# Kernel tuning notes

Measured on AMD Instinct MI355X. Metric: run time of the kernel, lower is better.

Reference implementation:

```python
import jax, jax.numpy as jnp
import numpy as np

DIM = 512; NH = 8; HD = DIM // NH; WS = 28; N = WS * WS; H3 = (DIM * 4) // 3; EPS = 1e-6; B = 16


def _rel_pos_index(H, W):
    # static numpy computation of Swin-style relative position index [N, N]
    coords = np.stack(np.meshgrid(np.arange(H), np.arange(W), indexing='ij')).reshape(2, -1)
    rel = (coords[:, :, None] - coords[:, None, :]).transpose(1, 2, 0)
    rel[..., 0] += H - 1
    rel[..., 1] += W - 1
    rel[..., 0] *= 2 * W - 1
    return rel.sum(-1)

RPI = jnp.asarray(_rel_pos_index(WS, WS))  # [N, N] int


def adaptive_ln(x, w, b, a1w, a1b, a2w, a2b):
    # x: [B,C,H,W]; adapt params from global-avg-pooled 1x1 convs (== matmuls)
    C = x.shape[1]
    pooled = x.mean(axis=(2, 3))                      # [B,C]
    h = jax.nn.relu(pooled @ a1w.T + a1b)             # [B,C/4]
    ad = h @ a2w.T + a2b                              # [B,2C]
    aw = ad[:, :C][:, :, None, None]
    ab = ad[:, C:][:, :, None, None]
    u = x.mean(axis=1, keepdims=True)
    s = ((x - u) ** 2).mean(axis=1, keepdims=True)
    xn = (x - u) * jax.lax.rsqrt(s + EPS)
    return (w[None, :, None, None] * (1.0 + aw)) * xn + (b[None, :, None, None] + ab)


def dwconv(x, w, b):
    y = jax.lax.conv_general_dilated(x, w, (1, 1), 'SAME', feature_group_count=x.shape[1],
                                     dimension_numbers=('NCHW', 'OIHW', 'NCHW'))
    return y + b[None, :, None, None]


def conv1x1(x, w, b):
    return jnp.einsum('bchw,oc->bohw', x, w) + b[None, :, None, None]


def _forward(x, face_priors, n1_w, n1_b, n1_a1w, n1_a1b, n1_a2w, n1_a2b,
             n2_w, n2_b, n2_a1w, n2_a1b, n2_a2w, n2_a2b,
             qkv_w, qkv_b, rpb_table, struct_prior, proj_w, proj_b,
             eye_w, eye_b, nose_w, nose_b, mouth_w, mouth_b,
             fusion_w, fusion_b, gate1_w, gate1_b, gate2_w, gate2_b,
             es1_w, es1_b, es2_w, es2_b, em1_w, em1_b, em2_w, em2_b,
             el1_w, el1_b, el2_w, el2_b, router_w, router_b):
    Bx, C, H, W = x.shape
    n = H * W
    shortcut = x
    xa = adaptive_ln(x, n1_w, n1_b, n1_a1w, n1_a1b, n1_a2w, n1_a2b)
    # --- TripletFaceAttention ---
    xf = xa.reshape(Bx, C, n).transpose(0, 2, 1)                     # [B,N,C]
    qkv = (xf @ qkv_w.T + qkv_b).reshape(Bx, n, 3, NH, HD).transpose(2, 0, 3, 1, 4)
    q, k, v = qkv[0], qkv[1], qkv[2]                                 # [B,h,N,d]
    attn = jnp.einsum('bhnd,bhmd->bhnm', q, k) * (HD ** -0.5)
    attn = attn + struct_prior                                       # learned structure prior [1,h,N,N]
    rpb = rpb_table[RPI]                                             # [N,N,h]
    attn = attn + jnp.transpose(rpb, (2, 0, 1))[None]                # + relative position bias
    attn = attn * face_priors[:, None]                               # multiplicative face mask
    attn = jax.nn.softmax(attn, axis=-1)
    o = jnp.einsum('bhnm,bhmd->bhnd', attn, v).transpose(0, 2, 1, 3).reshape(Bx, n, C)
    o = o @ proj_w.T + proj_b
    x = shortcut + o.transpose(0, 2, 1).reshape(Bx, C, H, W)
    # --- FaceTokenMixer ---
    xn2 = adaptive_ln(x, n2_w, n2_b, n2_a1w, n2_a1b, n2_a2w, n2_a2b)
    cat = jnp.concatenate([dwconv(xn2, eye_w, eye_b),
                           dwconv(xn2, nose_w, nose_b),
                           dwconv(xn2, mouth_w, mouth_b)], axis=1)   # [B,3C,H,W]
    g = jax.nn.sigmoid(conv1x1(jax.nn.relu(conv1x1(xn2, gate1_w, gate1_b)), gate2_w, gate2_b))
    x = x + conv1x1(cat * g, fusion_w, fusion_b)
    # --- EfficientMLP (3-expert MoE, soft routing) ---
    r = jax.nn.softmax(x.mean(axis=(2, 3)) @ router_w.T + router_b, axis=-1)  # [B,3]
    def expert(w1, b1, w2, b2):
        return conv1x1(jax.nn.gelu(conv1x1(x, w1, b1), approximate=False), w2, b2)
    out = (r[:, 0, None, None, None] * expert(es1_w, es1_b, es2_w, es2_b)
           + r[:, 1, None, None, None] * expert(em1_w, em1_b, em2_w, em2_b)
           + r[:, 2, None, None, None] * expert(el1_w, el1_b, el2_w, el2_b))
    return x + out


def setup_inputs() -> dict:
    ks = iter(jax.random.split(jax.random.key(0), 64))
    def rn(shape, s=0.02):
        return jax.random.normal(next(ks), shape, jnp.float32) * s
    d = {}
    d['x'] = jax.random.normal(next(ks), (B, DIM, WS, WS), jnp.float32)
    d['face_priors'] = jax.random.uniform(next(ks), (B, N, N), jnp.float32)
    for p in ('n1', 'n2'):
        d[p + '_w'] = jnp.ones((DIM,), jnp.float32)
        d[p + '_b'] = jnp.zeros((DIM,), jnp.float32)
        d[p + '_a1w'] = rn((DIM // 4, DIM)); d[p + '_a1b'] = jnp.zeros((DIM // 4,), jnp.float32)
        d[p + '_a2w'] = rn((2 * DIM, DIM // 4)); d[p + '_a2b'] = jnp.zeros((2 * DIM,), jnp.float32)
    d['qkv_w'] = rn((3 * DIM, DIM)); d['qkv_b'] = jnp.zeros((3 * DIM,), jnp.float32)
    d['rpb_table'] = rn(((2 * WS - 1) ** 2, NH))
    d['struct_prior'] = rn((1, NH, N, N))
    d['proj_w'] = rn((DIM, DIM)); d['proj_b'] = jnp.zeros((DIM,), jnp.float32)
    d['eye_w'] = rn((DIM, 1, 3, 3)); d['eye_b'] = jnp.zeros((DIM,), jnp.float32)
    d['nose_w'] = rn((DIM, 1, 5, 5)); d['nose_b'] = jnp.zeros((DIM,), jnp.float32)
    d['mouth_w'] = rn((DIM, 1, 7, 7)); d['mouth_b'] = jnp.zeros((DIM,), jnp.float32)
    d['fusion_w'] = rn((DIM, 3 * DIM)); d['fusion_b'] = jnp.zeros((DIM,), jnp.float32)
    d['gate1_w'] = rn((DIM // 4, DIM)); d['gate1_b'] = jnp.zeros((DIM // 4,), jnp.float32)
    d['gate2_w'] = rn((3 * DIM, DIM // 4)); d['gate2_b'] = jnp.zeros((3 * DIM,), jnp.float32)
    for e in ('es', 'em', 'el'):
        d[e + '1_w'] = rn((H3, DIM)); d[e + '1_b'] = jnp.zeros((H3,), jnp.float32)
        d[e + '2_w'] = rn((DIM, H3)); d[e + '2_b'] = jnp.zeros((DIM,), jnp.float32)
    d['router_w'] = rn((3, DIM)); d['router_b'] = jnp.zeros((3,), jnp.float32)
    return d


def reference(x, face_priors, n1_w, n1_b, n1_a1w, n1_a1b, n1_a2w, n1_a2b,
              n2_w, n2_b, n2_a1w, n2_a1b, n2_a2w, n2_a2b,
              qkv_w, qkv_b, rpb_table, struct_prior, proj_w, proj_b,
              eye_w, eye_b, nose_w, nose_b, mouth_w, mouth_b,
              fusion_w, fusion_b, gate1_w, gate1_b, gate2_w, gate2_b,
              es1_w, es1_b, es2_w, es2_b, em1_w, em1_b, em2_w, em2_b,
              el1_w, el1_b, el2_w, el2_b, router_w, router_b):
    return _forward(x, face_priors, n1_w, n1_b, n1_a1w, n1_a1b, n1_a2w, n1_a2b,
                    n2_w, n2_b, n2_a1w, n2_a1b, n2_a2w, n2_a2b,
                    qkv_w, qkv_b, rpb_table, struct_prior, proj_w, proj_b,
                    eye_w, eye_b, nose_w, nose_b, mouth_w, mouth_b,
                    fusion_w, fusion_b, gate1_w, gate1_b, gate2_w, gate2_b,
                    es1_w, es1_b, es2_w, es2_b, em1_w, em1_b, em2_w, em2_b,
                    el1_w, el1_b, el2_w, el2_b, router_w, router_b)
```

## Files before the change

### kernel.cpp

```cpp
#include <hip/hip_runtime.h>
#include <math.h>


#define NPIX 784
#define CDIM 512
#define NHEAD 8
#define C3 1536

typedef unsigned int uint;
typedef unsigned short ushort;
typedef float f32x4 __attribute__((ext_vector_type(4)));
typedef __bf16 bf16x8 __attribute__((ext_vector_type(8)));
typedef __bf16 bf16x2 __attribute__((ext_vector_type(2)));

#define OFF_XPM ((size_t)0)
#define OFF_W   ((size_t)3211264)
#define OFF_R2  ((size_t)5324288)
#define OFF_VBF ((size_t)14958080)
#define OFF_OBF ((size_t)18169344)
#define OFF_X2  ((size_t)21380608)
#define OFF_X3  ((size_t)27803136)
#define OFF_PL  ((size_t)34225664)
#define OFF_AD  ((size_t)34233856)
#define OFF_RB  ((size_t)34250240)
#define OFF_US  ((size_t)34250288)
#define OFF_RS  ((size_t)34262832)
#define OFF_E2C ((size_t)34275392)

#define WOFF_QKV 0
#define WOFF_PROJ 786432
#define WOFF_G1  1048576
#define WOFF_G2  1114112
#define WOFF_FUS 1310720
#define WOFF_E1  2097152

__device__ __forceinline__ ushort f2bf(float f) {
  __bf16 h = (__bf16)f;
  return __builtin_bit_cast(ushort, h);
}
__device__ __forceinline__ unsigned pack2bf(float lo, float hi) {
  bf16x2 v = {(__bf16)lo, (__bf16)hi};
  return __builtin_bit_cast(unsigned, v);
}
__device__ __forceinline__ float bf2f(ushort u) {
  unsigned x = ((unsigned)u) << 16;
  return __builtin_bit_cast(float, x);
}
__device__ __forceinline__ void unpack4bf(uint2 v, float* o) {
  o[0] = bf2f((ushort)(v.x & 0xffffu)); o[1] = bf2f((ushort)(v.x >> 16));
  o[2] = bf2f((ushort)(v.y & 0xffffu)); o[3] = bf2f((ushort)(v.y >> 16));
}

__global__ __launch_bounds__(64) void pool_mean_k(const float* __restrict__ x,
                                                  float* __restrict__ pooled) {
  int c = blockIdx.x, b = blockIdx.y;
  const float* row = x + ((size_t)b * CDIM + c) * NPIX;
  float s = 0.f;
  for (int i = threadIdx.x; i < NPIX; i += 64) s += row[i];
  #pragma unroll
  for (int off = 32; off; off >>= 1) s += __shfl_down(s, off);
  if (threadIdx.x == 0) pooled[b * CDIM + c] = s * (1.f / NPIX);
}

__global__ __launch_bounds__(256) void adapt_mlp_k(const float* __restrict__ pooled,
                                                   const float* __restrict__ a1w,
                                                   const float* __restrict__ a1b,
                                                   const float* __restrict__ a2w,
                                                   const float* __restrict__ a2b,
                                                   float* __restrict__ ad) {
  int b = blockIdx.x, tid = threadIdx.x;
  __shared__ float pl[CDIM];
  __shared__ float hh[128];
  for (int i = tid; i < CDIM; i += 256) pl[i] = pooled[b * CDIM + i];
  __syncthreads();
  if (tid < 128) {
    const float* w = a1w + (size_t)tid * CDIM;
    float a = a1b[tid];
    for (int k = 0; k < CDIM; ++k) a += w[k] * pl[k];
    hh[tid] = fmaxf(a, 0.f);
  }
  __syncthreads();
  for (int o = tid; o < 1024; o += 256) {
    const float* w = a2w + (size_t)o * 128;
    float a = a2b[o];
    for (int k = 0; k < 128; ++k) a += w[k] * hh[k];
    ad[b * 1024 + o] = a;
  }
}

template <int STATS>
__global__ __launch_bounds__(256) void ln_pm_k(const float* __restrict__ x,
                                               const float* __restrict__ w,
                                               const float* __restrict__ bias,
                                               const float* __restrict__ ad,
                                               ushort* __restrict__ out,
                                               float* __restrict__ ust,
                                               float* __restrict__ rstp) {
  int b = blockIdx.y;
  int p0 = blockIdx.x * 32;
  int tid = threadIdx.x;
  int px = tid & 31, cg = tid >> 5;
  int p = p0 + px;
  bool valid = p < NPIX;
  const float* xb = x + (size_t)b * CDIM * NPIX;
  float s = 0.f, s2 = 0.f;
  if (valid) {
    for (int c = cg * 64; c < cg * 64 + 64; ++c) {
      float v = xb[(size_t)c * NPIX + p];
      s += v; s2 += v * v;
    }
  }
  __shared__ float rs[8][32], rq[8][32], us[32], vs[32];
  rs[cg][px] = s; rq[cg][px] = s2;
  __syncthreads();
  if (tid < 32) {
    float ts = 0.f, ts2 = 0.f;
    #pragma unroll
    for (int g = 0; g < 8; ++g) { ts += rs[g][tid]; ts2 += rq[g][tid]; }
    float u = ts * (1.f / CDIM);
    float var = ts2 * (1.f / CDIM) - u * u;
    float rv = rsqrtf(var + 1e-6f);
    us[tid] = u; vs[tid] = rv;
    if (STATS && p0 + tid < NPIX) {
      ust[(size_t)b * NPIX + p0 + tid] = u;
      rstp[(size_t)b * NPIX + p0 + tid] = rv;
    }
  }
  __syncthreads();
  if (valid) {
    float u = us[px], rv = vs[px];
    const float* aw = ad + (size_t)b * 1024;
    const float* ab = aw + CDIM;
    ushort* ob = out + ((size_t)(b * NPIX + p)) * CDIM + cg * 64;
    for (int cb = 0; cb < 64; cb += 8) {
      int c = cg * 64 + cb;
      float vv[8];
      #pragma unroll
      for (int q = 0; q < 8; ++q) {
        float v = xb[(size_t)(c + q) * NPIX + p];
        vv[q] = w[c + q] * (1.f + aw[c + q]) * ((v - u) * rv) + (bias[c + q] + ab[c + q]);
      }
      uint4 o = {pack2bf(vv[0], vv[1]), pack2bf(vv[2], vv[3]),
                 pack2bf(vv[4], vv[5]), pack2bf(vv[6], vv[7])};
      *(uint4*)(ob + cb) = o;
    }
  }
}

struct CvtDesc {
  const float* s[11];
  ushort* d[11];
  int rows[11], sk[11], dk[11], ds[11], rr[11];
};
__global__ __launch_bounds__(256) void cvt_w_k(CvtDesc D) {
  int seg = blockIdx.y;
  int sk = D.sk[seg], dk = D.dk[seg], ds = D.ds[seg], rr = D.rr[seg];
  int total = D.rows[seg] * dk;
  const float* s = D.s[seg];
  ushort* d = D.d[seg];
  for (int i = blockIdx.x * 256 + threadIdx.x; i < total; i += gridDim.x * 256) {
    int r = i / dk, cc = i - r * dk;
    d[(size_t)r * ds + cc] = (cc < sk && r < rr) ? f2bf(s[(size_t)r * sk + cc]) : (ushort)0;
  }
}

__global__ __launch_bounds__(256) void sprpb_k(const float* __restrict__ sp,
                                               const float* __restrict__ rpb,
                                               ushort* __restrict__ out) {
  const int q = blockIdx.x, h = blockIdx.y;
  const int i1 = q / 28, j1 = q - i1 * 28;
  const float* src = sp + ((size_t)h * NPIX + q) * NPIX;
  ushort* dst = out + ((size_t)h * NPIX + q) * NPIX;
  for (int m = threadIdx.x; m < NPIX; m += 256) {
    int i2 = m / 28, j2 = m - i2 * 28;
    float rv = rpb[(size_t)((i1 - i2 + 27) * 55 + (j1 - j2 + 27)) * NHEAD + h];
    dst[m] = f2bf(src[m] + rv);
  }
}

__global__ __launch_bounds__(256) void fpcvt_k(const float* __restrict__ fp,
                                               ushort* __restrict__ out) {
  size_t i = (size_t)blockIdx.x * 256 + threadIdx.x;
  float4 v = *((const float4*)fp + i);
  ushort4 o;
  o.x = f2bf(v.x); o.y = f2bf(v.y); o.z = f2bf(v.z); o.w = f2bf(v.w);
  *((ushort4*)out + i) = o;
}

__global__ __launch_bounds__(512) void biaseff_k(const float* __restrict__ rbuf,
                                                 const float* __restrict__ b0,
                                                 const float* __restrict__ b1,
                                                 const float* __restrict__ b2,
                                                 const float* __restrict__ a0,
                                                 const float* __restrict__ a1,
                                                 const float* __restrict__ a2,
                                                 float* __restrict__ be,
                                                 float* __restrict__ e1bcat) {
  int b = blockIdx.x;
  if (b < 16) {
    int n = threadIdx.x;
    be[b * 512 + n] = rbuf[b * 3] * b0[n] + rbuf[b * 3 + 1] * b1[n] + rbuf[b * 3 + 2] * b2[n];
  } else {
    for (int i = threadIdx.x; i < 2112; i += 512) {
      int e = i / 704, r = i - e * 704;
      e1bcat[i] = (r < 682) ? (e == 0 ? a0 : e == 1 ? a1 : a2)[r] : 0.f;
    }
  }
}

template <int ORIENT, int EPI>
__global__ __launch_bounds__(256) void mgemm_k(const ushort* __restrict__ X,
                                               const ushort* __restrict__ Wt,
                                               const float* __restrict__ bias,
                                               const float* __restrict__ resid,
                                               const float* __restrict__ scales,
                                               void* __restrict__ OutV,
                                               int Ks, int Nreal, int Nstore) {
  const int bid = blockIdx.x;
  const int xcd = bid & 7;
  const int i = bid >> 3;
  const int mt_local = i % 14;
  const int nt = i / 14;
  const int m0 = (xcd * 14 + mt_local) * 112;
  const int n0 = nt * 128;
  const int bb = m0 / NPIX;
  const int t = threadIdx.x;
  const int w = t >> 6, lane = t & 63, c = lane & 15, g = lane >> 4;
  __shared__ ushort Xs[7168];
  __shared__ ushort Ws[8192];
  f32x4 acc[7][2];
  #pragma unroll
  for (int mi = 0; mi < 7; ++mi)
    #pragma unroll
    for (int ni = 0; ni < 2; ++ni) acc[mi][ni] = (f32x4){0.f, 0.f, 0.f, 0.f};

  for (int k0 = 0; k0 < Ks; k0 += 64) {
    for (int ii = t; ii < 896; ii += 256) {
      int m = ii >> 3, kg = ii & 7;
      uint4 v = *(const uint4*)(X + (size_t)(m0 + m) * Ks + k0 + kg * 8);
      *(uint4*)&Xs[m * 64 + ((kg ^ (m & 7)) << 3)] = v;
    }
    for (int ii = t; ii < 1024; ii += 256) {
      int n = ii >> 3, kg = ii & 7;
      uint4 v = {0u, 0u, 0u, 0u};
      if (n0 + n < Nreal) v = *(const uint4*)(Wt + (size_t)(n0 + n) * Ks + k0 + kg * 8);
      *(uint4*)&Ws[n * 64 + ((kg ^ (n & 7)) << 3)] = v;
    }
    __syncthreads();
    #pragma unroll
    for (int kc = 0; kc < 2; ++kc) {
      bf16x8 xf[7], wf[2];
      #pragma unroll
      for (int mi = 0; mi < 7; ++mi) {
        int m = mi * 16 + c;
        xf[mi] = *(const bf16x8*)&Xs[m * 64 + (((kc * 4 + g) ^ (m & 7)) << 3)];
      }
      #pragma unroll
      for (int ni = 0; ni < 2; ++ni) {
        int n = w * 32 + ni * 16 + c;
        wf[ni] = *(const bf16x8*)&Ws[n * 64 + (((kc * 4 + g) ^ (n & 7)) << 3)];
      }
      #pragma unroll
      for (int mi = 0; mi < 7; ++mi)
        #pragma unroll
        for (int ni = 0; ni < 2; ++ni)
          acc[mi][ni] = (ORIENT == 0)
            ? __builtin_amdgcn_mfma_f32_16x16x32_bf16(wf[ni], xf[mi], acc[mi][ni], 0, 0, 0)
            : __builtin_amdgcn_mfma_f32_16x16x32_bf16(xf[mi], wf[ni], acc[mi][ni], 0, 0, 0);
    }
    __syncthreads();
  }

  if (ORIENT == 0) {
    ushort* Ob = (ushort*)OutV;
    const int nbq = n0 + w * 32;
    float bi[2][4];
    #pragma unroll
    for (int ni = 0; ni < 2; ++ni)
      #pragma unroll
      for (int j = 0; j < 4; ++j) {
        int n = nbq + ni * 16 + g * 4 + j;
        bi[ni][j] = (n < Nreal) ? bias[n] : 0.f;
      }
    #pragma unroll
    for (int mi = 0; mi < 7; ++mi) {
      int m = m0 + mi * 16 + c;
      #pragma unroll
      for (int ni = 0; ni < 2; ++ni) {
        int nb = nbq + ni * 16 + g * 4;
        if (nb >= Nstore) continue;
        float v[4];
        #pragma unroll
        for (int j = 0; j < 4; ++j) v[j] = acc[mi][ni][j] + bi[ni][j];
        if (EPI == 1) {
          #pragma unroll
          for (int j = 0; j < 4; ++j) v[j] = fmaxf(v[j], 0.f);
        } else if (EPI == 2) {
          #pragma unroll
          for (int j = 0; j < 4; ++j)
            v[j] = 0.5f * v[j] * (1.f + erff(v[j] * 0.70710678118654752f));
        } else if (EPI == 3) {
          uint2 cm = *(const uint2*)&Ob[(size_t)m * Nstore + nb];
          float cf[4];
          unpack4bf(cm, cf);
          #pragma unroll
          for (int j = 0; j < 4; ++j)
            v[j] = (1.f / (1.f + __expf(-v[j]))) * cf[j];
        } else if (EPI == 5) {
          int e = nb / 704; e = (e > 2) ? 2 : e;
          float sc = scales[bb * 3 + e];
          #pragma unroll
          for (int j = 0; j < 4; ++j)
            v[j] = 0.5f * v[j] * (1.f + erff(v[j] * 0.70710678118654752f)) * sc;
        }
        uint2 o = {pack2bf(v[0], v[1]), pack2bf(v[2], v[3])};
        *(uint2*)&Ob[(size_t)m * Nstore + nb] = o;
      }
    }
  } else {
    const int prow = m0 - bb * NPIX;
    float* Ob = (float*)OutV + (size_t)bb * CDIM * NPIX;
    const float* Rb = resid + (size_t)bb * CDIM * NPIX;
    float sc = (EPI == 4 && scales) ? scales[bb * 3] : 1.f;
    #pragma unroll
    for (int ni = 0; ni < 2; ++ni) {
      int n = n0 + w * 32 + ni * 16 + c;
      float bv = (EPI == 5) ? bias[(size_t)bb * CDIM + n] : bias[n];
      #pragma unroll
      for (int mi = 0; mi < 7; ++mi) {
        int p = prow + mi * 16 + g * 4;
        size_t off = (size_t)n * NPIX + p;
        float4 r = *(const float4*)&Rb[off];
        f32x4 a = acc[mi][ni];
        float4 o = {r.x + sc * (a[0] + bv), r.y + sc * (a[1] + bv),
                    r.z + sc * (a[2] + bv), r.w + sc * (a[3] + bv)};
        *(float4*)&Ob[off] = o;
      }
    }
  }
}

__global__ __launch_bounds__(256) void vtr_k(const ushort* __restrict__ qkvbf,
                                             ushort* __restrict__ vbf) {
  const int p0 = blockIdx.x * 64, c0 = blockIdx.y * 64, b = blockIdx.z;
  __shared__ ushort T[64][72];
  for (int idx = threadIdx.x; idx < 512; idx += 256) {
    int pl = idx >> 3, cq = idx & 7;
    int p = p0 + pl;
    uint4 v = {0u, 0u, 0u, 0u};
    if (p < NPIX)
      v = *(const uint4*)(qkvbf + (size_t)(b * NPIX + p) * C3 + 1024 + c0 + cq * 8);
    *(uint4*)&T[pl][cq * 8] = v;
  }
  __syncthreads();
  for (int idx = threadIdx.x; idx < 512; idx += 256) {
    int cl = idx >> 3, pq = idx & 7;
    if (p0 + pq * 8 < NPIX) {
      ushort tmp[8];
      #pragma unroll
      for (int i = 0; i < 8; ++i) tmp[i] = T[pq * 8 + i][cl];
      *(uint4*)(vbf + ((size_t)(b * CDIM + c0 + cl)) * NPIX + p0 + pq * 8) =
          *(const uint4*)&tmp[0];
    }
  }
}

__global__ __launch_bounds__(256) void tr_cvt_k(const float* __restrict__ src,
                                                ushort* __restrict__ dst) {
  const int p0 = blockIdx.x * 64, c0 = blockIdx.y * 64, b = blockIdx.z;
  __shared__ ushort T[64][72];
  const float* sb = src + (size_t)b * CDIM * NPIX;
  for (int idx = threadIdx.x; idx < 4096; idx += 256) {
    int ci = idx >> 6, pj = idx & 63;
    int p = p0 + pj;
    T[pj][ci] = (p < NPIX) ? f2bf(sb[(size_t)(c0 + ci) * NPIX + p]) : (ushort)0;
  }
  __syncthreads();
  for (int idx = threadIdx.x; idx < 512; idx += 256) {
    int pj = idx >> 3, cq = idx & 7;
    int p = p0 + pj;
    if (p < NPIX) {
      uint4 v = *(const uint4*)&T[pj][cq * 8];
      *(uint4*)(dst + ((size_t)(b * NPIX + p)) * CDIM + c0 + cq * 8) = v;
    }
  }
}

__global__ __launch_bounds__(256) void attn_mfma_k(const ushort* __restrict__ qkvbf,
                                                   const ushort* __restrict__ vbf,
                                                   const ushort* __restrict__ sprpb,
                                                   const ushort* __restrict__ fpb,
                                                   ushort* __restrict__ obf) {
  const int bid = blockIdx.x;
  const int xcd = bid & 7;
  const int i = bid >> 3;
  const int b = xcd + 8 * (i / 56);
  const int r = i % 56;
  const int h = r & 7;
  const int qt = r >> 3;
  const int w = threadIdx.x >> 6, lane = threadIdx.x & 63;
  const int g = lane >> 4, c = lane & 15;
  const int q0 = qt * 128 + w * 32;
  if (q0 >= NPIX) return;
  const bool hasB = (q0 + 16) < NPIX;
  const int qA = q0 + c;
  const int qB = q0 + 16 + c;

  __shared__ uint BL[4][2][384];
  uint* bwA = BL[w][0];
  uint* bwB = BL[w][1];

  const ushort* qpA = qkvbf + (size_t)(b * NPIX + qA) * C3 + h * 64 + g * 8;
  const bf16x8 qfA0 = *(const bf16x8*)qpA;
  const bf16x8 qfA1 = *(const bf16x8*)(qpA + 32);
  bf16x8 qfB0 = qfA0, qfB1 = qfA1;
  if (hasB) {
    const ushort* qpB = qkvbf + (size_t)(b * NPIX + qB) * C3 + h * 64 + g * 8;
    qfB0 = *(const bf16x8*)qpB;
    qfB1 = *(const bf16x8*)(qpB + 32);
  }

  const ushort* kbase = qkvbf + (size_t)b * NPIX * C3 + 512 + h * 64 + g * 8;
  const ushort* vbase = vbf + ((size_t)b * CDIM + h * 64) * NPIX;
  const ushort* sprA = sprpb + ((size_t)h * NPIX + qA) * NPIX;
  const ushort* sprB = sprpb + ((size_t)h * NPIX + (hasB ? qB : qA)) * NPIX;
  const ushort* fpA = fpb + ((size_t)b * NPIX + qA) * NPIX;
  const ushort* fpB = fpb + ((size_t)b * NPIX + (hasB ? qB : qA)) * NPIX;

  f32x4 oA0 = {0.f, 0.f, 0.f, 0.f}, oA1 = oA0, oA2 = oA0, oA3 = oA0;
  f32x4 oB0 = oA0, oB1 = oA0, oB2 = oA0, oB3 = oA0;
  float MA = -1e30f, LA = 0.f, MB = -1e30f, LB = 0.f;

  for (int ms = 0; ms < 25; ++ms) {
    const int m0 = ms * 32;
    const bool full = (ms < 24);

    const ushort* kp = kbase + (size_t)(m0 + c) * C3;
    bf16x8 ka0 = *(const bf16x8*)kp;
    bf16x8 ka1 = *(const bf16x8*)(kp + 32);
    bf16x8 kb0 = ka0, kb1 = ka1;
    if (full) {
      const ushort* kp1 = kp + (size_t)16 * C3;
      kb0 = *(const bf16x8*)kp1;
      kb1 = *(const bf16x8*)(kp1 + 32);
    }

    f32x4 sA0 = {0.f, 0.f, 0.f, 0.f}, sA1 = sA0;
    sA0 = __builtin_amdgcn_mfma_f32_16x16x32_bf16(ka0, qfA0, sA0, 0, 0, 0);
    sA0 = __builtin_amdgcn_mfma_f32_16x16x32_bf16(ka1, qfA1, sA0, 0, 0, 0);
    if (full) {
      sA1 = __builtin_amdgcn_mfma_f32_16x16x32_bf16(kb0, qfA0, sA1, 0, 0, 0);
      sA1 = __builtin_amdgcn_mfma_f32_16x16x32_bf16(kb1, qfA1, sA1, 0, 0, 0);
    }

    float vA0[4], vA1[4];
    {
      float spv[4], fpv[4];
      unpack4bf(*(const uint2*)(sprA + m0 + g * 4), spv);
      unpack4bf(*(const uint2*)(fpA + m0 + g * 4), fpv);
      #pragma unroll
      for (int j = 0; j < 4; ++j) vA0[j] = fmaf(sA0[j], 0.125f, spv[j]) * fpv[j];
      if (full) {
        unpack4bf(*(const uint2*)(sprA + m0 + 16 + g * 4), spv);
        unpack4bf(*(const uint2*)(fpA + m0 + 16 + g * 4), fpv);
        #pragma unroll
        for (int j = 0; j < 4; ++j) vA1[j] = fmaf(sA1[j], 0.125f, spv[j]) * fpv[j];
      }
    }
    {
      float tm = fmaxf(fmaxf(vA0[0], vA0[1]), fmaxf(vA0[2], vA0[3]));
      if (full) tm = fmaxf(tm, fmaxf(fmaxf(vA1[0], vA1[1]), fmaxf(vA1[2], vA1[3])));
      tm = fmaxf(tm, __shfl_xor(tm, 16));
      tm = fmaxf(tm, __shfl_xor(tm, 32));
      if (__any(tm > MA)) {
        const float nM = fmaxf(MA, tm);
        const float fac = __expf(MA - nM);
        LA *= fac;
        #pragma unroll
        for (int j = 0; j < 4; ++j) { oA0[j] *= fac; oA1[j] *= fac; oA2[j] *= fac; oA3[j] *= fac; }
        MA = nM;
      }
      float p0v[4], p1v[4];
      float ps = 0.f;
      #pragma unroll
      for (int j = 0; j < 4; ++j) { p0v[j] = __expf(vA0[j] - MA); ps += p0v[j]; }
      if (full) {
        #pragma unroll
        for (int j = 0; j < 4; ++j) { p1v[j] = __expf(vA1[j] - MA); ps += p1v[j]; }
      }
      ps += __shfl_xor(ps, 16);
      ps += __shfl_xor(ps, 32);
      LA += ps;
      uint2 wlo, whi;
      wlo.x = pack2bf(p0v[0], p0v[1]);
      wlo.y = pack2bf(p0v[2], p0v[3]);
      whi.x = full ? pack2bf(p1v[0], p1v[1]) : 0u;
      whi.y = full ? pack2bf(p1v[2], p1v[3]) : 0u;
      *(uint2*)&bwA[lane * 6] = wlo;
      *(uint2*)&bwA[lane * 6 + 2] = whi;
    }

    if (hasB) {
      f32x4 sB0 = {0.f, 0.f, 0.f, 0.f}, sB1 = sB0;
      sB0 = __builtin_amdgcn_mfma_f32_16x16x32_bf16(ka0, qfB0, sB0, 0, 0, 0);
      sB0 = __builtin_amdgcn_mfma_f32_16x16x32_bf16(ka1, qfB1, sB0, 0, 0, 0);
      if (full) {
        sB1 = __builtin_amdgcn_mfma_f32_16x16x32_bf16(kb0, qfB0, sB1, 0, 0, 0);
        sB1 = __builtin_amdgcn_mfma_f32_16x16x32_bf16(kb1, qfB1, sB1, 0, 0, 0);
      }
      float vB0[4], vB1[4];
      {
        float spv[4], fpv[4];
        unpack4bf(*(const uint2*)(sprB + m0 + g * 4), spv);
        unpack4bf(*(const uint2*)(fpB + m0 + g * 4), fpv);
        #pragma unroll
        for (int j = 0; j < 4; ++j) vB0[j] = fmaf(sB0[j], 0.125f, spv[j]) * fpv[j];
        if (full) {
          unpack4bf(*(const uint2*)(sprB + m0 + 16 + g * 4), spv);
          unpack4bf(*(const uint2*)(fpB + m0 + 16 + g * 4), fpv);
          #pragma unroll
          for (int j = 0; j < 4; ++j) vB1[j] = fmaf(sB1[j], 0.125f, spv[j]) * fpv[j];
        }
      }
      float tm = fmaxf(fmaxf(vB0[0], vB0[1]), fmaxf(vB0[2], vB0[3]));
      if (full) tm = fmaxf(tm, fmaxf(fmaxf(vB1[0], vB1[1]), fmaxf(vB1[2], vB1[3])));
      tm = fmaxf(tm, __shfl_xor(tm, 16));
      tm = fmaxf(tm, __shfl_xor(tm, 32));
      if (__any(tm > MB)) {
        const float nM = fmaxf(MB, tm);
        const float fac = __expf(MB - nM);
        LB *= fac;
        #pragma unroll
        for (int j = 0; j < 4; ++j) { oB0[j] *= fac; oB1[j] *= fac; oB2[j] *= fac; oB3[j] *= fac; }
        MB = nM;
      }
      float p0v[4], p1v[4];
      float ps = 0.f;
      #pragma unroll
      for (int j = 0; j < 4; ++j) { p0v[j] = __expf(vB0[j] - MB); ps += p0v[j]; }
      if (full) {
        #pragma unroll
        for (int j = 0; j < 4; ++j) { p1v[j] = __expf(vB1[j] - MB); ps += p1v[j]; }
      }
      ps += __shfl_xor(ps, 16);
      ps += __shfl_xor(ps, 32);
      LB += ps;
      uint2 wlo, whi;
      wlo.x = pack2bf(p0v[0], p0v[1]);
      wlo.y = pack2bf(p0v[2], p0v[3]);
      whi.x = full ? pack2bf(p1v[0], p1v[1]) : 0u;
      whi.y = full ? pack2bf(p1v[2], p1v[3]) : 0u;
      *(uint2*)&bwB[lane * 6] = wlo;
      *(uint2*)&bwB[lane * 6 + 2] = whi;
    }

    const int f = g >> 1;
    const int slo = 32 * (g & 1) + c;
    uint2 blo = *(const uint2*)&bwA[slo * 6 + f * 2];
    uint2 bhi = *(const uint2*)&bwA[(slo + 16) * 6 + f * 2];
    uint4 bba = {blo.x, blo.y, bhi.x, bhi.y};
    const bf16x8 pfA = __builtin_bit_cast(bf16x8, bba);

    const ushort* vp = vbase + (size_t)c * NPIX + m0 + g * 8;
    bf16x8 vf0 = *(const bf16x8*)(vp);
    bf16x8 vf1 = *(const bf16x8*)(vp + (size_t)16 * NPIX);
    bf16x8 vf2 = *(const bf16x8*)(vp + (size_t)32 * NPIX);
    bf16x8 vf3 = *(const bf16x8*)(vp + (size_t)48 * NPIX);
    oA0 = __builtin_amdgcn_mfma_f32_16x16x32_bf16(vf0, pfA, oA0, 0, 0, 0);
    oA1 = __builtin_amdgcn_mfma_f32_16x16x32_bf16(vf1, pfA, oA1, 0, 0, 0);
    oA2 = __builtin_amdgcn_mfma_f32_16x16x32_bf16(vf2, pfA, oA2, 0, 0, 0);
    oA3 = __builtin_amdgcn_mfma_f32_16x16x32_bf16(vf3, pfA, oA3, 0, 0, 0);
    if (hasB) {
      uint2 clo = *(const uint2*)&bwB[slo * 6 + f * 2];
      uint2 chi = *(const uint2*)&bwB[(slo + 16) * 6 + f * 2];
      uint4 bbb = {clo.x, clo.y, chi.x, chi.y};
      const bf16x8 pfB = __builtin_bit_cast(bf16x8, bbb);
      oB0 = __builtin_amdgcn_mfma_f32_16x16x32_bf16(vf0, pfB, oB0, 0, 0, 0);
      oB1 = __builtin_amdgcn_mfma_f32_16x16x32_bf16(vf1, pfB, oB1, 0, 0, 0);
      oB2 = __builtin_amdgcn_mfma_f32_16x16x32_bf16(vf2, pfB, oB2, 0, 0, 0);
      oB3 = __builtin_amdgcn_mfma_f32_16x16x32_bf16(vf3, pfB, oB3, 0, 0, 0);
    }
  }

  {
    const float invL = 1.f / LA;
    ushort* dst = obf + (size_t)(b * NPIX + qA) * CDIM + h * 64 + g * 4;
    f32x4 ot[4] = {oA0, oA1, oA2, oA3};
    #pragma unroll
    for (int t2 = 0; t2 < 4; ++t2) {
      uint2 o = {pack2bf(ot[t2][0] * invL, ot[t2][1] * invL),
                 pack2bf(ot[t2][2] * invL, ot[t2][3] * invL)};
      *(uint2*)(dst + t2 * 16) = o;
    }
  }
  if (hasB) {
    const float invL = 1.f / LB;
    ushort* dst = obf + (size_t)(b * NPIX + qB) * CDIM + h * 64 + g * 4;
    f32x4 ot[4] = {oB0, oB1, oB2, oB3};
    #pragma unroll
    for (int t2 = 0; t2 < 4; ++t2) {
      uint2 o = {pack2bf(ot[t2][0] * invL, ot[t2][1] * invL),
                 pack2bf(ot[t2][2] * invL, ot[t2][3] * invL)};
      *(uint2*)(dst + t2 * 16) = o;
    }
  }
}

__device__ __forceinline__ float bf2f_s(ushort u) { return bf2f(u); }

template <int R>
__device__ __forceinline__ void conv_pass(const ushort* __restrict__ plane_ci,
                                          const float* __restrict__ wl_ci,
                                          float bv, int slot,
                                          ushort (*__restrict__ outb)[16], int ci) {
  constexpr int K = 2 * R + 1;
  float wreg[K * K];
  #pragma unroll
  for (int i = 0; i < K * K; ++i) wreg[i] = wl_ci[i];
  #pragma unroll
  for (int r7 = 0; r7 < 7; ++r7) {
    const int run = slot + r7 * 16;
    const int y = run >> 2, x0 = (run & 3) * 7;
    float acc[7];
    #pragma unroll
    for (int i = 0; i < 7; ++i) acc[i] = bv;
    #pragma unroll
    for (int dy = 0; dy < K; ++dy) {
      const ushort* rp = plane_ci + (y + 3 - R + dy) * 34 + (x0 + 3 - R);
      float win[7 + 2 * R];
      #pragma unroll
      for (int k = 0; k < 7 + 2 * R; ++k) win[k] = bf2f_s(rp[k]);
      #pragma unroll
      for (int i = 0; i < 7; ++i)
        #pragma unroll
        for (int k = 0; k < K; ++k)
          acc[i] = fmaf(win[i + k], wreg[dy * K + k], acc[i]);
    }
    #pragma unroll
    for (int i = 0; i < 7; ++i) outb[y * 28 + x0 + i][ci] = f2bf(acc[i]);
  }
}

__global__ __launch_bounds__(256) void dwln_k(const float* __restrict__ x2,
    const float* __restrict__ ust, const float* __restrict__ rst,
    const float* __restrict__ ad, const float* __restrict__ n2w,
    const float* __restrict__ n2b,
    const float* __restrict__ ew, const float* __restrict__ eb,
    const float* __restrict__ nw, const float* __restrict__ nb,
    const float* __restrict__ mw, const float* __restrict__ mb,
    ushort* __restrict__ cat) {
  const int cg = blockIdx.x, b = blockIdx.y;
  const int c0 = cg * 16;
  const int t = threadIdx.x;
  const int ci = t & 15, slot = t >> 4;

  __shared__ ushort plane[16][1156];
  __shared__ ushort outb[784][16];
  __shared__ float Wl[16 * 49];
  __shared__ float LWs[16], LBs[16];

  {
    uint* pz = (uint*)&plane[0][0];
    for (int i = t; i < 16 * 1156 / 2; i += 256) pz[i] = 0u;
  }
  if (t < 16) {
    int cc = c0 + t;
    float aw = ad[b * 1024 + cc], ab = ad[b * 1024 + 512 + cc];
    LWs[t] = n2w[cc] * (1.f + aw);
    LBs[t] = n2b[cc] + ab;
  }
  __syncthreads();

  {
    float uu[4], rr[4];
    #pragma unroll
    for (int j = 0; j < 4; ++j) {
      int p = t + j * 256;
      if (p < NPIX) {
        uu[j] = ust[(size_t)b * NPIX + p];
        rr[j] = rst[(size_t)b * NPIX + p];
      }
    }
    for (int cc = 0; cc < 16; ++cc) {
      const float* xp = x2 + ((size_t)(b * CDIM + c0 + cc)) * NPIX;
      float lw = LWs[cc], lb = LBs[cc];
      #pragma unroll
      for (int j = 0; j < 4; ++j) {
        int p = t + j * 256;
        if (p < NPIX) {
          int y = p / 28, xx2 = p - y * 28;
          plane[cc][(y + 3) * 34 + xx2 + 3] = f2bf(lw * (xp[p] - uu[j]) * rr[j] + lb);
        }
      }
    }
  }
  __syncthreads();

  #pragma unroll 1
  for (int cv = 0; cv < 3; ++cv) {
    const float* gw = (cv == 0) ? ew : (cv == 1) ? nw : mw;
    const float* gb = (cv == 0) ? eb : (cv == 1) ? nb : mb;
    const int K2 = (cv == 0) ? 9 : (cv == 1) ? 25 : 49;
    for (int i = t; i < 16 * K2; i += 256) {
      int cc = i / K2, k = i - cc * K2;
      Wl[cc * K2 + k] = gw[(size_t)(c0 + cc) * K2 + k];
    }
    __syncthreads();
    float bv = gb[c0 + ci];
    if (cv == 0)      conv_pass<1>(&plane[ci][0], &Wl[ci * 9],  bv, slot, outb, ci);
    else if (cv == 1) conv_pass<2>(&plane[ci][0], &Wl[ci * 25], bv, slot, outb, ci);
    else              conv_pass<3>(&plane[ci][0], &Wl[ci * 49], bv, slot, outb, ci);
    __syncthreads();
    for (int idx = t; idx < NPIX * 2; idx += 256) {
      int p = idx >> 1, half = idx & 1;
      uint4 v = *(const uint4*)&outb[p][half * 8];
      *(uint4*)(cat + ((size_t)(b * NPIX + p)) * C3 + cv * 512 + c0 + half * 8) = v;
    }
    __syncthreads();
  }
}

__global__ __launch_bounds__(64) void router_k(const float* __restrict__ pooled,
                                               const float* __restrict__ rw,
                                               const float* __restrict__ rb,
                                               float* __restrict__ r) {
  int b = blockIdx.x, lane = threadIdx.x;
  float a0 = 0.f, a1 = 0.f, a2 = 0.f;
  for (int k = lane; k < CDIM; k += 64) {
    float p = pooled[b * CDIM + k];
    a0 += rw[k] * p;
    a1 += rw[CDIM + k] * p;
    a2 += rw[2 * CDIM + k] * p;
  }
  #pragma unroll
  for (int off = 32; off; off >>= 1) {
    a0 += __shfl_down(a0, off);
    a1 += __shfl_down(a1, off);
    a2 += __shfl_down(a2, off);
  }
  if (lane == 0) {
    float l0 = a0 + rb[0], l1 = a1 + rb[1], l2 = a2 + rb[2];
    float mx = fmaxf(l0, fmaxf(l1, l2));
    float e0 = __expf(l0 - mx), e1 = __expf(l1 - mx), e2 = __expf(l2 - mx);
    float inv = 1.f / (e0 + e1 + e2);
    r[b * 3 + 0] = e0 * inv;
    r[b * 3 + 1] = e1 * inv;
    r[b * 3 + 2] = e2 * inv;
  }
}

extern "C" void kernel_launch(void* const* d_in, const int* in_sizes, int n_in,
                              void* d_out, int out_size, void* d_ws, size_t ws_size,
                              hipStream_t stream) {
  (void)in_sizes; (void)n_in; (void)out_size; (void)ws_size;
  const float* x         = (const float*)d_in[0];
  const float* fpri      = (const float*)d_in[1];
  const float* n1_w      = (const float*)d_in[2];
  const float* n1_b      = (const float*)d_in[3];
  const float* n1_a1w    = (const float*)d_in[4];
  const float* n1_a1b    = (const float*)d_in[5];
  const float* n1_a2w    = (const float*)d_in[6];
  const float* n1_a2b    = (const float*)d_in[7];
  const float* n2_w      = (const float*)d_in[8];
  const float* n2_b      = (const float*)d_in[9];
  const float* n2_a1w    = (const float*)d_in[10];
  const float* n2_a1b    = (const float*)d_in[11];
  const float* n2_a2w    = (const float*)d_in[12];
  const float* n2_a2b    = (const float*)d_in[13];
  const float* qkv_w     = (const float*)d_in[14];
  const float* qkv_b     = (const float*)d_in[15];
  const float* rpb_table = (const float*)d_in[16];
  const float* sprior    = (const float*)d_in[17];
  const float* proj_w    = (const float*)d_in[18];
  const float* proj_b    = (const float*)d_in[19];
  const float* eye_w     = (const float*)d_in[20];
  const float* eye_b     = (const float*)d_in[21];
  const float* nose_w    = (const float*)d_in[22];
  const float* nose_b    = (const float*)d_in[23];
  const float* mouth_w   = (const float*)d_in[24];
  const float* mouth_b   = (const float*)d_in[25];
  const float* fusion_w  = (const float*)d_in[26];
  const float* fusion_b  = (const float*)d_in[27];
  const float* gate1_w   = (const float*)d_in[28];
  const float* gate1_b   = (const float*)d_in[29];
  const float* gate2_w   = (const float*)d_in[30];
  const float* gate2_b   = (const float*)d_in[31];
  const float* e1w[3] = {(const float*)d_in[32], (const float*)d_in[36], (const float*)d_in[40]};
  const float* e1b[3] = {(const float*)d_in[33], (const float*)d_in[37], (const float*)d_in[41]};
  const float* e2w[3] = {(const float*)d_in[34], (const float*)d_in[38], (const float*)d_in[42]};
  const float* e2b[3] = {(const float*)d_in[35], (const float*)d_in[39], (const float*)d_in[43]};
  const float* router_w  = (const float*)d_in[44];
  const float* router_b  = (const float*)d_in[45];

  float* ws    = (float*)d_ws;
  ushort* xpm  = (ushort*)(ws + OFF_XPM);
  ushort* wb   = (ushort*)(ws + OFF_W);
  ushort* r2u  = (ushort*)(ws + OFF_R2);
  ushort* vbf  = (ushort*)(ws + OFF_VBF);
  ushort* obf  = (ushort*)(ws + OFF_OBF);
  float* x2    = ws + OFF_X2;
  float* x3    = ws + OFF_X3;
  float* pld   = ws + OFF_PL;
  float* adb   = ws + OFF_AD;
  float* rbuf  = ws + OFF_RB;
  float* ust   = ws + OFF_US;
  float* rst   = ws + OFF_RS;
  float* outp  = (float*)d_out;

  ushort* qkvw  = wb + WOFF_QKV;
  ushort* projw = wb + WOFF_PROJ;
  ushort* g1w   = wb + WOFF_G1;
  ushort* g2w   = wb + WOFF_G2;
  ushort* fusw  = wb + WOFF_FUS;
  ushort* e1cat = wb + WOFF_E1;
  ushort* e2cat = (ushort*)(ws + OFF_E2C);
  float* be     = adb;
  float* e1bcat = adb + 8192;

  ushort* fpbf   = (ushort*)x2;
  ushort* sprpbf = (ushort*)x3;

  CvtDesc D;
  auto seg = [&](int s2, const float* src, ushort* dst, int rows, int sk, int dk,
                 int ds, int rr) {
    D.s[s2] = src; D.d[s2] = dst; D.rows[s2] = rows; D.sk[s2] = sk;
    D.dk[s2] = dk; D.ds[s2] = ds; D.rr[s2] = rr;
  };
  seg(0, qkv_w,    qkvw,  1536, 512,  512,  512,  1536);
  seg(1, proj_w,   projw, 512,  512,  512,  512,  512);
  seg(2, gate1_w,  g1w,   128,  512,  512,  512,  128);
  seg(3, gate2_w,  g2w,   1536, 128,  128,  128,  1536);
  seg(4, fusion_w, fusw,  512,  1536, 1536, 1536, 512);
  for (int e = 0; e < 3; ++e) {
    seg(5 + e, e1w[e], e1cat + (size_t)e * 704 * 512, 704, 512, 512, 512, 682);
    seg(8 + e, e2w[e], e2cat + (size_t)e * 704,       512, 682, 704, 2112, 512);
  }
  cvt_w_k<<<dim3(512, 11), 256, 0, stream>>>(D);

  sprpb_k<<<dim3(NPIX, NHEAD), 256, 0, stream>>>(sprior, rpb_table, sprpbf);
  fpcvt_k<<<9604, 256, 0, stream>>>(fpri, fpbf);

  pool_mean_k<<<dim3(CDIM, 16), 64, 0, stream>>>(x, pld);
  adapt_mlp_k<<<16, 256, 0, stream>>>(pld, n1_a1w, n1_a1b, n1_a2w, n1_a2b, adb);
  ln_pm_k<0><<<dim3(25, 16), 256, 0, stream>>>(x, n1_w, n1_b, adb, xpm, nullptr, nullptr);

  mgemm_k<0, 0><<<1344, 256, 0, stream>>>(xpm, qkvw, qkv_b, nullptr, nullptr,
                                          r2u, 512, 1536, 1536);
  vtr_k<<<dim3(13, 8, 16), 256, 0, stream>>>(r2u, vbf);
  attn_mfma_k<<<896, 256, 0, stream>>>(r2u, vbf, sprpbf, fpbf, obf);
  mgemm_k<1, 4><<<448, 256, 0, stream>>>(obf, projw, proj_b, x, nullptr,
                                         x2, 512, 512, 512);

  pool_mean_k<<<dim3(CDIM, 16), 64, 0, stream>>>(x2, pld);
  adapt_mlp_k<<<16, 256, 0, stream>>>(pld, n2_a1w, n2_a1b, n2_a2w, n2_a2b, adb);
  ln_pm_k<1><<<dim3(25, 16), 256, 0, stream>>>(x2, n2_w, n2_b, adb, xpm, ust, rst);
  dwln_k<<<dim3(32, 16), 256, 0, stream>>>(x2, ust, rst, adb, n2_w, n2_b,
                                           eye_w, eye_b, nose_w, nose_b, mouth_w, mouth_b,
                                           r2u);
  mgemm_k<0, 1><<<112, 256, 0, stream>>>(xpm, g1w, gate1_b, nullptr, nullptr,
                                         obf, 512, 128, 128);
  mgemm_k<0, 3><<<1344, 256, 0, stream>>>(obf, g2w, gate2_b, nullptr, nullptr,
                                          r2u, 128, 1536, 1536);
  mgemm_k<1, 4><<<448, 256, 0, stream>>>(r2u, fusw, fusion_b, x2, nullptr,
                                         x3, 1536, 512, 512);

  tr_cvt_k<<<dim3(13, 8, 16), 256, 0, stream>>>(x3, xpm);
  pool_mean_k<<<dim3(CDIM, 16), 64, 0, stream>>>(x3, pld);
  router_k<<<16, 64, 0, stream>>>(pld, router_w, router_b, rbuf);
  biaseff_k<<<17, 512, 0, stream>>>(rbuf, e2b[0], e2b[1], e2b[2],
                                    e1b[0], e1b[1], e1b[2], be, e1bcat);
  mgemm_k<0, 5><<<1904, 256, 0, stream>>>(xpm, e1cat, e1bcat, nullptr, rbuf,
                                          r2u, 512, 2112, 2112);
  mgemm_k<1, 5><<<448, 256, 0, stream>>>(r2u, e2cat, be, x3, nullptr,
                                         outp, 2112, 512, 512);
}
```

Measured before the change: 816.7 us.

## Fuse pooling and bf16 transpose into GEMM epilogues; prefetch attention operands

```diff
diff --git a/kernel.cpp b/kernel.cpp
--- a/kernel.cpp
+++ b/kernel.cpp
@@ -59,7 +59,7 @@
   for (int i = threadIdx.x; i < NPIX; i += 64) s += row[i];
   #pragma unroll
   for (int off = 32; off; off >>= 1) s += __shfl_down(s, off);
-  if (threadIdx.x == 0) pooled[b * CDIM + c] = s * (1.f / NPIX);
+  if (threadIdx.x == 0) pooled[b * CDIM + c] = s;
 }
 
 __global__ __launch_bounds__(256) void adapt_mlp_k(const float* __restrict__ pooled,
@@ -71,7 +71,8 @@
   int b = blockIdx.x, tid = threadIdx.x;
   __shared__ float pl[CDIM];
   __shared__ float hh[128];
-  for (int i = tid; i < CDIM; i += 256) pl[i] = pooled[b * CDIM + i];
+  for (int i = tid; i < CDIM; i += 256)
+    pl[i] = pooled[b * CDIM + i] * (1.f / NPIX);
   __syncthreads();
   if (tid < 128) {
     const float* w = a1w + (size_t)tid * CDIM;
@@ -208,13 +209,15 @@
   }
 }
 
-template <int ORIENT, int EPI>
+template <int ORIENT, int EPI, int POOL, int DUALBF>
 __global__ __launch_bounds__(256) void mgemm_k(const ushort* __restrict__ X,
                                                const ushort* __restrict__ Wt,
                                                const float* __restrict__ bias,
                                                const float* __restrict__ resid,
                                                const float* __restrict__ scales,
                                                void* __restrict__ OutV,
+                                               float* __restrict__ pool_out,
+                                               ushort* __restrict__ pm_out,
                                                int Ks, int Nreal, int Nstore) {
   const int bid = blockIdx.x;
   const int xcd = bid & 7;
@@ -326,6 +329,7 @@
     for (int ni = 0; ni < 2; ++ni) {
       int n = n0 + w * 32 + ni * 16 + c;
       float bv = (EPI == 5) ? bias[(size_t)bb * CDIM + n] : bias[n];
+      float cs = 0.f;
       #pragma unroll
       for (int mi = 0; mi < 7; ++mi) {
         int p = prow + mi * 16 + g * 4;
@@ -335,6 +339,19 @@
         float4 o = {r.x + sc * (a[0] + bv), r.y + sc * (a[1] + bv),
                     r.z + sc * (a[2] + bv), r.w + sc * (a[3] + bv)};
         *(float4*)&Ob[off] = o;
+        if (POOL) cs += o.x + o.y + o.z + o.w;
+        if (DUALBF) {
+          size_t mg = (size_t)(m0 + mi * 16 + g * 4);
+          pm_out[mg * CDIM + n] = f2bf(o.x);
+          pm_out[(mg + 1) * CDIM + n] = f2bf(o.y);
+          pm_out[(mg + 2) * CDIM + n] = f2bf(o.z);
+          pm_out[(mg + 3) * CDIM + n] = f2bf(o.w);
+        }
+      }
+      if (POOL) {
+        cs += __shfl_xor(cs, 16);
+        cs += __shfl_xor(cs, 32);
+        if (g == 0) atomicAdd(pool_out + (size_t)bb * CDIM + n, cs);
       }
     }
   }
@@ -365,26 +382,9 @@
   }
 }
 
-__global__ __launch_bounds__(256) void tr_cvt_k(const float* __restrict__ src,
-                                                ushort* __restrict__ dst) {
-  const int p0 = blockIdx.x * 64, c0 = blockIdx.y * 64, b = blockIdx.z;
-  __shared__ ushort T[64][72];
-  const float* sb = src + (size_t)b * CDIM * NPIX;
-  for (int idx = threadIdx.x; idx < 4096; idx += 256) {
-    int ci = idx >> 6, pj = idx & 63;
-    int p = p0 + pj;
-    T[pj][ci] = (p < NPIX) ? f2bf(sb[(size_t)(c0 + ci) * NPIX + p]) : (ushort)0;
-  }
-  __syncthreads();
-  for (int idx = threadIdx.x; idx < 512; idx += 256) {
-    int pj = idx >> 3, cq = idx & 7;
-    int p = p0 + pj;
-    if (p < NPIX) {
-      uint4 v = *(const uint4*)&T[pj][cq * 8];
-      *(uint4*)(dst + ((size_t)(b * NPIX + p)) * CDIM + c0 + cq * 8) = v;
-    }
-  }
-}
+struct KFr { bf16x8 a0, a1, b0, b1; };
+struct VFr { bf16x8 v0, v1, v2, v3; };
+struct BFr { uint2 sl, fl, sh, fh; };
 
 __global__ __launch_bounds__(256) void attn_mfma_k(const ushort* __restrict__ qkvbf,
                                                    const ushort* __restrict__ vbf,
@@ -427,47 +427,77 @@
   const ushort* fpA = fpb + ((size_t)b * NPIX + qA) * NPIX;
   const ushort* fpB = fpb + ((size_t)b * NPIX + (hasB ? qB : qA)) * NPIX;
 
+  auto load_k = [&](int m0, bool tfull) -> KFr {
+    KFr k;
+    const ushort* kp = kbase + (size_t)(m0 + c) * C3;
+    k.a0 = *(const bf16x8*)kp;
+    k.a1 = *(const bf16x8*)(kp + 32);
+    const ushort* kp1 = kp + (tfull ? (size_t)16 * C3 : 0);
+    k.b0 = *(const bf16x8*)kp1;
+    k.b1 = *(const bf16x8*)(kp1 + 32);
+    return k;
+  };
+  auto load_v = [&](int m0) -> VFr {
+    VFr v;
+    const ushort* vp = vbase + (size_t)c * NPIX + m0 + g * 8;
+    v.v0 = *(const bf16x8*)(vp);
+    v.v1 = *(const bf16x8*)(vp + (size_t)16 * NPIX);
+    v.v2 = *(const bf16x8*)(vp + (size_t)32 * NPIX);
+    v.v3 = *(const bf16x8*)(vp + (size_t)48 * NPIX);
+    return v;
+  };
+  auto load_b = [&](const ushort* spr, const ushort* fp, int m0) -> BFr {
+    BFr x;
+    x.sl = *(const uint2*)(spr + m0 + g * 4);
+    x.fl = *(const uint2*)(fp + m0 + g * 4);
+    x.sh = *(const uint2*)(spr + m0 + 16 + g * 4);
+    x.fh = *(const uint2*)(fp + m0 + 16 + g * 4);
+    return x;
+  };
+
   f32x4 oA0 = {0.f, 0.f, 0.f, 0.f}, oA1 = oA0, oA2 = oA0, oA3 = oA0;
   f32x4 oB0 = oA0, oB1 = oA0, oB2 = oA0, oB3 = oA0;
   float MA = -1e30f, LA = 0.f, MB = -1e30f, LB = 0.f;
 
+  KFr kc = load_k(0, true);
+  VFr vc = load_v(0);
+  BFr bcA = load_b(sprA, fpA, 0);
+  BFr bcB = bcA;
+  if (hasB) bcB = load_b(sprB, fpB, 0);
+
   for (int ms = 0; ms < 25; ++ms) {
     const int m0 = ms * 32;
     const bool full = (ms < 24);
 
-    const ushort* kp = kbase + (size_t)(m0 + c) * C3;
-    bf16x8 ka0 = *(const bf16x8*)kp;
-    bf16x8 ka1 = *(const bf16x8*)(kp + 32);
-    bf16x8 kb0 = ka0, kb1 = ka1;
+    KFr kn; VFr vn; BFr bnA, bnB;
     if (full) {
-      const ushort* kp1 = kp + (size_t)16 * C3;
-      kb0 = *(const bf16x8*)kp1;
-      kb1 = *(const bf16x8*)(kp1 + 32);
+      const int nm0 = m0 + 32;
+      kn = load_k(nm0, ms + 1 < 24);
+      vn = load_v(nm0);
+      bnA = load_b(sprA, fpA, nm0);
+      if (hasB) bnB = load_b(sprB, fpB, nm0);
     }
 
     f32x4 sA0 = {0.f, 0.f, 0.f, 0.f}, sA1 = sA0;
-    sA0 = __builtin_amdgcn_mfma_f32_16x16x32_bf16(ka0, qfA0, sA0, 0, 0, 0);
-    sA0 = __builtin_amdgcn_mfma_f32_16x16x32_bf16(ka1, qfA1, sA0, 0, 0, 0);
+    sA0 = __builtin_amdgcn_mfma_f32_16x16x32_bf16(kc.a0, qfA0, sA0, 0, 0, 0);
+    sA0 = __builtin_amdgcn_mfma_f32_16x16x32_bf16(kc.a1, qfA1, sA0, 0, 0, 0);
     if (full) {
-      sA1 = __builtin_amdgcn_mfma_f32_16x16x32_bf16(kb0, qfA0, sA1, 0, 0, 0);
-      sA1 = __builtin_amdgcn_mfma_f32_16x16x32_bf16(kb1, qfA1, sA1, 0, 0, 0);
-    }
-
-    float vA0[4], vA1[4];
+      sA1 = __builtin_amdgcn_mfma_f32_16x16x32_bf16(kc.b0, qfA0, sA1, 0, 0, 0);
+      sA1 = __builtin_amdgcn_mfma_f32_16x16x32_bf16(kc.b1, qfA1, sA1, 0, 0, 0);
+    }
     {
+      float vA0[4], vA1[4];
       float spv[4], fpv[4];
-      unpack4bf(*(const uint2*)(sprA + m0 + g * 4), spv);
-      unpack4bf(*(const uint2*)(fpA + m0 + g * 4), fpv);
+      unpack4bf(bcA.sl, spv);
+      unpack4bf(bcA.fl, fpv);
       #pragma unroll
       for (int j = 0; j < 4; ++j) vA0[j] = fmaf(sA0[j], 0.125f, spv[j]) * fpv[j];
       if (full) {
-        unpack4bf(*(const uint2*)(sprA + m0 + 16 + g * 4), spv);
-        unpack4bf(*(const uint2*)(fpA + m0 + 16 + g * 4), fpv);
+        unpack4bf(bcA.sh, spv);
+        unpack4bf(bcA.fh, fpv);
         #pragma unroll
         for (int j = 0; j < 4; ++j) vA1[j] = fmaf(sA1[j], 0.125f, spv[j]) * fpv[j];
       }
-    }
-    {
       float tm = fmaxf(fmaxf(vA0[0], vA0[1]), fmaxf(vA0[2], vA0[3]));
       if (full) tm = fmaxf(tm, fmaxf(fmaxf(vA1[0], vA1[1]), fmaxf(vA1[2], vA1[3])));
       tm = fmaxf(tm, __shfl_xor(tm, 16));
@@ -502,25 +532,23 @@
 
     if (hasB) {
       f32x4 sB0 = {0.f, 0.f, 0.f, 0.f}, sB1 = sB0;
-      sB0 = __builtin_amdgcn_mfma_f32_16x16x32_bf16(ka0, qfB0, sB0, 0, 0, 0);
-      sB0 = __builtin_amdgcn_mfma_f32_16x16x32_bf16(ka1, qfB1, sB0, 0, 0, 0);
+      sB0 = __builtin_amdgcn_mfma_f32_16x16x32_bf16(kc.a0, qfB0, sB0, 0, 0, 0);
+      sB0 = __builtin_amdgcn_mfma_f32_16x16x32_bf16(kc.a1, qfB1, sB0, 0, 0, 0);
       if (full) {
-        sB1 = __builtin_amdgcn_mfma_f32_16x16x32_bf16(kb0, qfB0, sB1, 0, 0, 0);
-        sB1 = __builtin_amdgcn_mfma_f32_16x16x32_bf16(kb1, qfB1, sB1, 0, 0, 0);
+        sB1 = __builtin_amdgcn_mfma_f32_16x16x32_bf16(kc.b0, qfB0, sB1, 0, 0, 0);
+        sB1 = __builtin_amdgcn_mfma_f32_16x16x32_bf16(kc.b1, qfB1, sB1, 0, 0, 0);
       }
       float vB0[4], vB1[4];
-      {
-        float spv[4], fpv[4];
-        unpack4bf(*(const uint2*)(sprB + m0 + g * 4), spv);
-        unpack4bf(*(const uint2*)(fpB + m0 + g * 4), fpv);
+      float spv[4], fpv[4];
+      unpack4bf(bcB.sl, spv);
+      unpack4bf(bcB.fl, fpv);
+      #pragma unroll
+      for (int j = 0; j < 4; ++j) vB0[j] = fmaf(sB0[j], 0.125f, spv[j]) * fpv[j];
+      if (full) {
+        unpack4bf(bcB.sh, spv);
+        unpack4bf(bcB.fh, fpv);
         #pragma unroll
-        for (int j = 0; j < 4; ++j) vB0[j] = fmaf(sB0[j], 0.125f, spv[j]) * fpv[j];
-        if (full) {
-          unpack4bf(*(const uint2*)(sprB + m0 + 16 + g * 4), spv);
-          unpack4bf(*(const uint2*)(fpB + m0 + 16 + g * 4), fpv);
-          #pragma unroll
-          for (int j = 0; j < 4; ++j) vB1[j] = fmaf(sB1[j], 0.125f, spv[j]) * fpv[j];
-        }
+        for (int j = 0; j < 4; ++j) vB1[j] = fmaf(sB1[j], 0.125f, spv[j]) * fpv[j];
       }
       float tm = fmaxf(fmaxf(vB0[0], vB0[1]), fmaxf(vB0[2], vB0[3]));
       if (full) tm = fmaxf(tm, fmaxf(fmaxf(vB1[0], vB1[1]), fmaxf(vB1[2], vB1[3])));
@@ -560,26 +588,22 @@
     uint2 bhi = *(const uint2*)&bwA[(slo + 16) * 6 + f * 2];
     uint4 bba = {blo.x, blo.y, bhi.x, bhi.y};
     const bf16x8 pfA = __builtin_bit_cast(bf16x8, bba);
-
-    const ushort* vp = vbase + (size_t)c * NPIX + m0 + g * 8;
-    bf16x8 vf0 = *(const bf16x8*)(vp);
-    bf16x8 vf1 = *(const bf16x8*)(vp + (size_t)16 * NPIX);
-    bf16x8 vf2 = *(const bf16x8*)(vp + (size_t)32 * NPIX);
-    bf16x8 vf3 = *(const bf16x8*)(vp + (size_t)48 * NPIX);
-    oA0 = __builtin_amdgcn_mfma_f32_16x16x32_bf16(vf0, pfA, oA0, 0, 0, 0);
-    oA1 = __builtin_amdgcn_mfma_f32_16x16x32_bf16(vf1, pfA, oA1, 0, 0, 0);
-    oA2 = __builtin_amdgcn_mfma_f32_16x16x32_bf16(vf2, pfA, oA2, 0, 0, 0);
-    oA3 = __builtin_amdgcn_mfma_f32_16x16x32_bf16(vf3, pfA, oA3, 0, 0, 0);
+    oA0 = __builtin_amdgcn_mfma_f32_16x16x32_bf16(vc.v0, pfA, oA0, 0, 0, 0);
+    oA1 = __builtin_amdgcn_mfma_f32_16x16x32_bf16(vc.v1, pfA, oA1, 0, 0, 0);
+    oA2 = __builtin_amdgcn_mfma_f32_16x16x32_bf16(vc.v2, pfA, oA2, 0, 0, 0);
+    oA3 = __builtin_amdgcn_mfma_f32_16x16x32_bf16(vc.v3, pfA, oA3, 0, 0, 0);
     if (hasB) {
       uint2 clo = *(const uint2*)&bwB[slo * 6 + f * 2];
       uint2 chi = *(const uint2*)&bwB[(slo + 16) * 6 + f * 2];
       uint4 bbb = {clo.x, clo.y, chi.x, chi.y};
       const bf16x8 pfB = __builtin_bit_cast(bf16x8, bbb);
-      oB0 = __builtin_amdgcn_mfma_f32_16x16x32_bf16(vf0, pfB, oB0, 0, 0, 0);
-      oB1 = __builtin_amdgcn_mfma_f32_16x16x32_bf16(vf1, pfB, oB1, 0, 0, 0);
-      oB2 = __builtin_amdgcn_mfma_f32_16x16x32_bf16(vf2, pfB, oB2, 0, 0, 0);
-      oB3 = __builtin_amdgcn_mfma_f32_16x16x32_bf16(vf3, pfB, oB3, 0, 0, 0);
-    }
+      oB0 = __builtin_amdgcn_mfma_f32_16x16x32_bf16(vc.v0, pfB, oB0, 0, 0, 0);
+      oB1 = __builtin_amdgcn_mfma_f32_16x16x32_bf16(vc.v1, pfB, oB1, 0, 0, 0);
+      oB2 = __builtin_amdgcn_mfma_f32_16x16x32_bf16(vc.v2, pfB, oB2, 0, 0, 0);
+      oB3 = __builtin_amdgcn_mfma_f32_16x16x32_bf16(vc.v3, pfB, oB3, 0, 0, 0);
+    }
+
+    if (full) { kc = kn; vc = vn; bcA = bnA; if (hasB) bcB = bnB; }
   }
 
   {
@@ -727,7 +751,7 @@
   int b = blockIdx.x, lane = threadIdx.x;
   float a0 = 0.f, a1 = 0.f, a2 = 0.f;
   for (int k = lane; k < CDIM; k += 64) {
-    float p = pooled[b * CDIM + k];
+    float p = pooled[b * CDIM + k] * (1.f / NPIX);
     a0 += rw[k] * p;
     a1 += rw[CDIM + k] * p;
     a2 += rw[2 * CDIM + k] * p;
@@ -844,33 +868,32 @@
   adapt_mlp_k<<<16, 256, 0, stream>>>(pld, n1_a1w, n1_a1b, n1_a2w, n1_a2b, adb);
   ln_pm_k<0><<<dim3(25, 16), 256, 0, stream>>>(x, n1_w, n1_b, adb, xpm, nullptr, nullptr);
 
-  mgemm_k<0, 0><<<1344, 256, 0, stream>>>(xpm, qkvw, qkv_b, nullptr, nullptr,
-                                          r2u, 512, 1536, 1536);
+  mgemm_k<0, 0, 0, 0><<<1344, 256, 0, stream>>>(xpm, qkvw, qkv_b, nullptr, nullptr,
+                                                r2u, nullptr, nullptr, 512, 1536, 1536);
   vtr_k<<<dim3(13, 8, 16), 256, 0, stream>>>(r2u, vbf);
   attn_mfma_k<<<896, 256, 0, stream>>>(r2u, vbf, sprpbf, fpbf, obf);
-  mgemm_k<1, 4><<<448, 256, 0, stream>>>(obf, projw, proj_b, x, nullptr,
-                                         x2, 512, 512, 512);
-
-  pool_mean_k<<<dim3(CDIM, 16), 64, 0, stream>>>(x2, pld);
+  hipMemsetAsync(pld, 0, 16 * CDIM * sizeof(float), stream);
+  mgemm_k<1, 4, 1, 0><<<448, 256, 0, stream>>>(obf, projw, proj_b, x, nullptr,
+                                               x2, pld, nullptr, 512, 512, 512);
+
   adapt_mlp_k<<<16, 256, 0, stream>>>(pld, n2_a1w, n2_a1b, n2_a2w, n2_a2b, adb);
   ln_pm_k<1><<<dim3(25, 16), 256, 0, stream>>>(x2, n2_w, n2_b, adb, xpm, ust, rst);
   dwln_k<<<dim3(32, 16), 256, 0, stream>>>(x2, ust, rst, adb, n2_w, n2_b,
                                            eye_w, eye_b, nose_w, nose_b, mouth_w, mouth_b,
                                            r2u);
-  mgemm_k<0, 1><<<112, 256, 0, stream>>>(xpm, g1w, gate1_b, nullptr, nullptr,
-                                         obf, 512, 128, 128);
-  mgemm_k<0, 3><<<1344, 256, 0, stream>>>(obf, g2w, gate2_b, nullptr, nullptr,
-                                          r2u, 128, 1536, 1536);
-  mgemm_k<1, 4><<<448, 256, 0, stream>>>(r2u, fusw, fusion_b, x2, nullptr,
-                                         x3, 1536, 512, 512);
-
-  tr_cvt_k<<<dim3(13, 8, 16), 256, 0, stream>>>(x3, xpm);
-  pool_mean_k<<<dim3(CDIM, 16), 64, 0, stream>>>(x3, pld);
+  mgemm_k<0, 1, 0, 0><<<112, 256, 0, stream>>>(xpm, g1w, gate1_b, nullptr, nullptr,
+                                               obf, nullptr, nullptr, 512, 128, 128);
+  mgemm_k<0, 3, 0, 0><<<1344, 256, 0, stream>>>(obf, g2w, gate2_b, nullptr, nullptr,
+                                                r2u, nullptr, nullptr, 128, 1536, 1536);
+  hipMemsetAsync(pld, 0, 16 * CDIM * sizeof(float), stream);
+  mgemm_k<1, 4, 1, 1><<<448, 256, 0, stream>>>(r2u, fusw, fusion_b, x2, nullptr,
+                                               x3, pld, xpm, 1536, 512, 512);
+
   router_k<<<16, 64, 0, stream>>>(pld, router_w, router_b, rbuf);
   biaseff_k<<<17, 512, 0, stream>>>(rbuf, e2b[0], e2b[1], e2b[2],
                                     e1b[0], e1b[1], e1b[2], be, e1bcat);
-  mgemm_k<0, 5><<<1904, 256, 0, stream>>>(xpm, e1cat, e1bcat, nullptr, rbuf,
-                                          r2u, 512, 2112, 2112);
-  mgemm_k<1, 5><<<448, 256, 0, stream>>>(r2u, e2cat, be, x3, nullptr,
-                                         outp, 2112, 512, 512);
-}
+  mgemm_k<0, 5, 0, 0><<<1904, 256, 0, stream>>>(xpm, e1cat, e1bcat, nullptr, rbuf,
+                                                r2u, nullptr, nullptr, 512, 2112, 2112);
+  mgemm_k<1, 5, 0, 0><<<448, 256, 0, stream>>>(r2u, e2cat, be, x3, nullptr,
+                                               outp, nullptr, nullptr, 2112, 512, 512);
+}
```

After: 787.7 us. 1.04x faster.
